# Optimization experiments

Hardware: AMD Instinct MI355X
Metric: run time of the kernel (lower is better)

Reference implementation:

```python
import jax, jax.numpy as jnp
import numpy as np
from jax import lax

C, CMID, RED, SCALE, KUP, KENC = 128, 64, 8, 2, 5, 3


def _conv(x, w, b=None, pad=0, groups=1):
    y = lax.conv_general_dilated(x, w, (1, 1), [(pad, pad), (pad, pad)],
                                 feature_group_count=groups,
                                 dimension_numbers=('NCHW', 'OIHW', 'NCHW'))
    if b is not None:
        y = y + b[None, :, None, None]
    return y


def setup_inputs() -> dict:
    key = jax.random.key(0)
    ks = jax.random.split(key, 8)
    s = 0.05
    return {
        'X': jax.random.normal(ks[0], (2, C, 64, 64), jnp.float32),
        'w3': jax.random.normal(ks[1], (CMID, C, 3, 3), jnp.float32) * s,
        'b3': jnp.zeros((CMID,), jnp.float32),
        'w5': jax.random.normal(ks[2], (CMID, C, 5, 5), jnp.float32) * s,
        'b5': jnp.zeros((CMID,), jnp.float32),
        'wa1': jax.random.normal(ks[3], (CMID // RED, CMID, 1, 1), jnp.float32) * s,
        'ba1': jnp.zeros((CMID // RED,), jnp.float32),
        'wa2': jax.random.normal(ks[4], (CMID, CMID // RED, 1, 1), jnp.float32) * s,
        'ba2': jnp.zeros((CMID,), jnp.float32),
        'wedge': jax.random.normal(ks[5], (CMID, 1, 3, 3), jnp.float32) * s,
        'wenc': jax.random.normal(ks[6], ((SCALE * KUP) ** 2, CMID, KENC, KENC), jnp.float32) * s,
    }


def reference(X, w3, b3, w5, b5, wa1, ba1, wa2, ba2, wedge, wenc):
    b, c, h, w = X.shape
    h_, w_ = h * SCALE, w * SCALE

    # kernel-prediction branch: 3x3 + 5x5 compression convs
    W = _conv(X, w3, b3, pad=1) + _conv(X, w5, b5, pad=2)

    # DetailEnhanceAttention: SE-style channel gate + depthwise edge conv
    avg = jnp.mean(W, axis=(2, 3), keepdims=True)            # (b, cmid, 1, 1)
    a = _conv(avg, wa1, ba1, pad=0)
    a = jax.nn.sigmoid(_conv(a, wa2, ba2, pad=0))
    edge = _conv(W, wedge, None, pad=1, groups=CMID)          # depthwise 3x3
    W = W * a + edge

    # encoder conv -> (b, (scale*k_up)^2, h, w)
    W = _conv(W, wenc, None, pad=KENC // 2)

    # PixelShuffle(scale): channels (k_up^2, r, r) -> (k_up^2, h*r, w*r)
    Wp = W.reshape(b, KUP * KUP, SCALE, SCALE, h, w)
    Wp = Wp.transpose(0, 1, 4, 2, 5, 3).reshape(b, KUP * KUP, h_, w_)
    Wp = jax.nn.softmax(Wp, axis=1)                           # softmax over k_up^2 taps

    # nearest upsample of X to (b, c, h_, w_)
    Xu = jnp.repeat(jnp.repeat(X, SCALE, axis=2), SCALE, axis=3)

    # unfold: kernel=k_up, dilation=scale, padding=k_up//2*scale
    p = (KUP // 2) * SCALE
    Xpad = jnp.pad(Xu, ((0, 0), (0, 0), (p, p), (p, p)))
    # (b, c, k_up^2, h_, w_), tap index = ki*k_up + kj (torch unfold order)
    patches = jnp.stack([
        Xpad[:, :, i * SCALE:i * SCALE + h_, j * SCALE:j * SCALE + w_]
        for i in range(KUP) for j in range(KUP)
    ], axis=2)

    out = jnp.einsum('bkhw,bckhw->bchw', Wp, patches)
    return out
```

## Files before the change

### kernel.cpp

```cpp
#include <hip/hip_runtime.h>
#include <math.h>

typedef __attribute__((ext_vector_type(2))) _Float16 f16x2;
typedef __attribute__((ext_vector_type(4))) _Float16 f16x4;
typedef __attribute__((ext_vector_type(8))) _Float16 f16x8;
typedef __attribute__((ext_vector_type(4))) float f32x4;

#if __has_builtin(__builtin_amdgcn_fdot2)
#define FDOT2(a, b, c) __builtin_amdgcn_fdot2((a), (b), (c), false)
#else
static __device__ __forceinline__ float FDOT2(f16x2 a, f16x2 b, float c) {
  return c + (float)a[0] * (float)b[0] + (float)a[1] * (float)b[1];
}
#endif

#define XPAD8_B  0
#define WFC_B    2506752
#define WFE_B    2916352
#define WFEATP_B 3045376
#define WEDGET_B 4194304
#define BCOMB_B  4195456
#define AVG_B    4195712

__global__ __launch_bounds__(256) void prep_kernel(
    const float* __restrict__ X,
    const float* __restrict__ w3, const float* __restrict__ b3,
    const float* __restrict__ w5, const float* __restrict__ b5,
    const float* __restrict__ wedge, const float* __restrict__ wenc,
    char* __restrict__ wsb) {
  int idx = blockIdx.x * 256 + threadIdx.x;
  if (idx < 156672) {
    int x = idx % 72;
    int t = idx / 72;
    int y = t % 68;
    int t2 = t / 68;
    int gg = t2 & 15, b = t2 >> 4;
    int yy = y - 2, xx = x - 2;
    bool ok = (yy >= 0 && yy < 64 && xx >= 0 && xx < 64);
    f16x8 h;
#pragma unroll
    for (int j = 0; j < 8; ++j) {
      float v = ok ? X[((b * 128 + gg * 8 + j) << 12) + yy * 64 + xx] : 0.f;
      h[j] = (_Float16)v;
    }
    ((f16x8*)(wsb + XPAD8_B))[idx] = h;
  }
  if (idx < 25600) {
    int l = idx & 63;
    int q = idx >> 6;
    int ntg = q & 3;
    int q2 = q >> 2;
    int cc = q2 & 3;
    int t = q2 >> 2;
    int ky = t / 5, kx = t % 5;
    int oc = ntg * 16 + (l & 15);
    int ci0 = cc * 32 + (l >> 4) * 8;
    f16x8 h;
#pragma unroll
    for (int i = 0; i < 8; ++i) {
      int ci = ci0 + i;
      float v = w5[(oc * 128 + ci) * 25 + t];
      if (ky >= 1 && ky <= 3 && kx >= 1 && kx <= 3)
        v += w3[(oc * 128 + ci) * 9 + (ky - 1) * 3 + (kx - 1)];
      h[i] = (_Float16)v;
    }
    ((f16x8*)(wsb + WFC_B))[idx] = h;
  }
  if (idx < 8064) {
    int l = idx & 63;
    int q = idx >> 6;
    int nt = q % 7;
    int q2 = q / 7;
    int cc = q2 & 1;
    int t = q2 >> 1;
    int oc = nt * 16 + (l & 15);
    int ci0 = cc * 32 + (l >> 4) * 8;
    f16x8 h;
#pragma unroll
    for (int i = 0; i < 8; ++i) {
      float v = (oc < 100) ? wenc[(oc * 64 + ci0 + i) * 9 + t] : 0.f;
      h[i] = (_Float16)v;
    }
    ((f16x8*)(wsb + WFE_B))[idx] = h;
  }
  if (idx < 6272) {
    int plane = idx / 392, p = idx % 392;
    int r, c;
    if (p < 136) {
      r = (p >= 68) ? 65 : 0;
      c = p % 68;
    } else {
      int q = p - 136;
      r = 1 + (q >> 2);
      int cm = q & 3;
      c = (cm == 0) ? 0 : (64 + cm);
    }
    f16x8 z = {(_Float16)0.f, (_Float16)0.f, (_Float16)0.f, (_Float16)0.f,
               (_Float16)0.f, (_Float16)0.f, (_Float16)0.f, (_Float16)0.f};
    *(f16x8*)((_Float16*)(wsb + WFEATP_B) + ((size_t)(plane * 66 + r) * 68 + c) * 8) = z;
  }
  if (idx < 72) {
    int k = idx >> 3, gg = idx & 7;
    f16x8 h;
#pragma unroll
    for (int j = 0; j < 8; ++j) h[j] = (_Float16)wedge[(gg * 8 + j) * 9 + k];
    ((f16x8*)(wsb + WEDGET_B))[idx] = h;
  }
  if (idx < 64) ((float*)(wsb + BCOMB_B))[idx] = b3[idx] + b5[idx];
  if (idx < 128) ((float*)(wsb + AVG_B))[idx] = b3[idx & 63] + b5[idx & 63];
}

__global__ __launch_bounds__(256) void convw_kernel(
    const _Float16* __restrict__ xpad8, const f16x8* __restrict__ wfc,
    const float* __restrict__ bcomb, _Float16* __restrict__ wfeatp,
    float* __restrict__ avg) {
  __shared__ __attribute__((aligned(16))) _Float16 xs[18560];
  __shared__ float red[64];
  const int tid = threadIdx.x;
  const int z = blockIdx.z;
  const int b = z >> 2, ntg = z & 3;
  const int tx0 = blockIdx.x * 8, ty0 = blockIdx.y * 8;

  for (int u = tid; u < 2304; u += 256) {
    int gg = u / 144;
    int rem = u - gg * 144;
    int r = rem / 12, c = rem - r * 12;
    f16x8 v = *(const f16x8*)&xpad8[((size_t)((b * 16 + gg) * 68 + ty0 + r) * 72 + tx0 + c) * 8];
    *(f16x8*)&xs[gg * 1160 + r * 96 + c * 8] = v;
  }
  __syncthreads();

  const int w = __builtin_amdgcn_readfirstlane(tid >> 6);
  const int l = tid & 63;
  const int lm = l & 15, lg = l >> 4;
  const int p = w * 16 + lm;
  const int abase = (p >> 3) * 96 + (p & 7) * 8;

  f32x4 accA = {0.f, 0.f, 0.f, 0.f}, accB = {0.f, 0.f, 0.f, 0.f};
  for (int dy = 0; dy < 5; ++dy) {
    for (int dx = 0; dx < 5; ++dx) {
      const int t = dy * 5 + dx;
      const int toff = abase + dy * 96 + dx * 8;
      const f16x8* wt = wfc + (t * 16 + ntg) * 64 + l;
#pragma unroll
      for (int cc = 0; cc < 4; ++cc) {
        f16x8 a = *(const f16x8*)&xs[(cc * 4 + lg) * 1160 + toff];
        f16x8 bb = wt[cc * 256];
        if (cc & 1)
          accB = __builtin_amdgcn_mfma_f32_16x16x32_f16(a, bb, accB, 0, 0, 0);
        else
          accA = __builtin_amdgcn_mfma_f32_16x16x32_f16(a, bb, accA, 0, 0, 0);
      }
    }
  }
  f32x4 acc = accA + accB;

  float s = acc[0] + acc[1] + acc[2] + acc[3];
  s += __shfl_xor(s, 16);
  s += __shfl_xor(s, 32);
  const float bias = bcomb[ntg * 16 + lm];
  __syncthreads();
#pragma unroll
  for (int r = 0; r < 4; ++r) {
    int pd = w * 16 + lg * 4 + r;
    xs[pd * 24 + lm] = (_Float16)(acc[r] + bias);
  }
  if (l < 16) red[w * 16 + lm] = s;
  __syncthreads();
  if (tid < 128) {
    int g2 = tid >> 6, pd = tid & 63;
    f16x8 v = *(const f16x8*)&xs[pd * 24 + g2 * 8];
    int gy = ty0 + (pd >> 3), gx = tx0 + (pd & 7);
    *(f16x8*)&wfeatp[((size_t)((b * 8 + ntg * 2 + g2) * 66 + 1 + gy) * 68 + 1 + gx) * 8] = v;
  }
  if (tid < 16) {
    float tot = red[tid] + red[16 + tid] + red[32 + tid] + red[48 + tid];
    atomicAdd(&avg[b * 64 + ntg * 16 + tid], tot * (1.f / 4096.f));
  }
}

#define SM_XT  0
#define SM_XSV 26880
#define SM_TS  34688
#define SM_SML 34688
#define SM_SMW 49536
#define SM_TOT 57216

__global__ __launch_bounds__(512) void enccarafe_kernel(
    const _Float16* __restrict__ wfeatp, const f16x8* __restrict__ wfe,
    const _Float16* __restrict__ xpad8, const f16x8* __restrict__ wedgeT,
    const float* __restrict__ wa1, const float* __restrict__ ba1,
    const float* __restrict__ wa2, const float* __restrict__ ba2,
    const float* __restrict__ avg, float* __restrict__ out) {
  __shared__ __attribute__((aligned(16))) char smem[SM_TOT];
  __shared__ f16x8 wedt[72];
  __shared__ float tlat[8];
  __shared__ float gsh[64];
  _Float16* xt = (_Float16*)(smem + SM_XT);
  _Float16* xsv = (_Float16*)(smem + SM_XSV);
  _Float16* ts = (_Float16*)(smem + SM_TS);
  float* sml = (float*)(smem + SM_SML);
  f16x2* smw2 = (f16x2*)(smem + SM_SMW);

  const int tid = threadIdx.x;
  const int b = blockIdx.z;
  const int tx0 = blockIdx.x * 8, ty0 = blockIdx.y * 4;

  for (int u = tid; u < 1664; u += 512) {
    int gg = u / 104;
    int rem = u - gg * 104;
    int r = rem / 13, c = rem - r * 13;
    f16x8 v = *(const f16x8*)&xpad8[((size_t)((b * 16 + gg) * 68 + ty0 + r) * 72 + tx0 + c) * 8];
    *(f16x8*)&xt[gg * 840 + r * 104 + c * 8] = v;
  }
  for (int u = tid; u < 768; u += 512) {
    int gg = u / 96;
    int rem = u - gg * 96;
    int r = rem / 12, c = rem - r * 12;
    int pr = ty0 - 1 + r, pc = tx0 - 1 + c;
    f16x8 v = {(_Float16)0.f, (_Float16)0.f, (_Float16)0.f, (_Float16)0.f,
               (_Float16)0.f, (_Float16)0.f, (_Float16)0.f, (_Float16)0.f};
    if (pr >= 0 && pr < 66 && pc >= 0 && pc < 68)
      v = *(const f16x8*)&wfeatp[((size_t)((b * 8 + gg) * 66 + pr) * 68 + pc) * 8];
    *(f16x8*)&ts[gg * 776 + r * 96 + c * 8] = v;
  }
  if (tid < 72) wedt[tid] = wedgeT[tid];
  if (tid < 8) {
    float s = ba1[tid];
    for (int i = 0; i < 64; ++i) s += wa1[tid * 64 + i] * avg[b * 64 + i];
    tlat[tid] = s;
  }
  __syncthreads();
  if (tid < 64) {
    float s = ba2[tid];
#pragma unroll
    for (int j = 0; j < 8; ++j) s += wa2[tid * 8 + j] * tlat[j];
    gsh[tid] = 1.f / (1.f + expf(-s));
  }
  __syncthreads();

  for (int u = tid; u < 480; u += 512) {
    int gg = u / 60;
    int rem = u - gg * 60;
    int r6 = rem / 10, c10 = rem - r6 * 10;
    int vy = ty0 - 1 + r6, vx = tx0 - 1 + c10;
    f16x8 res = {(_Float16)0.f, (_Float16)0.f, (_Float16)0.f, (_Float16)0.f,
                 (_Float16)0.f, (_Float16)0.f, (_Float16)0.f, (_Float16)0.f};
    if (vy >= 0 && vy < 64 && vx >= 0 && vx < 64) {
      float vout[8];
      f16x8 ctr = *(const f16x8*)&ts[gg * 776 + (r6 + 1) * 96 + (c10 + 1) * 8];
#pragma unroll
      for (int j = 0; j < 8; ++j) vout[j] = (float)ctr[j] * gsh[gg * 8 + j];
#pragma unroll
      for (int ky = 0; ky < 3; ++ky) {
#pragma unroll
        for (int kx = 0; kx < 3; ++kx) {
          int k = ky * 3 + kx;
          f16x8 tv = *(const f16x8*)&ts[gg * 776 + (r6 + ky) * 96 + (c10 + kx) * 8];
          f16x8 wv = wedt[k * 8 + gg];
#pragma unroll
          for (int j = 0; j < 8; ++j) vout[j] = fmaf((float)wv[j], (float)tv[j], vout[j]);
        }
      }
#pragma unroll
      for (int j = 0; j < 8; ++j) res[j] = (_Float16)vout[j];
    }
    *(f16x8*)&xsv[gg * 488 + r6 * 80 + c10 * 8] = res;
  }
  __syncthreads();

  {
    const int w = __builtin_amdgcn_readfirstlane(tid >> 6);
    const int l = tid & 63;
    const int pg = w & 1, hs = w >> 1;
    const int lm = l & 15, lg = l >> 4;
    const int p = pg * 16 + lm;
    const int abase = (p >> 3) * 80 + (p & 7) * 8;
    const int nt0 = hs * 2;
    const int ncnt = (hs == 3) ? 1 : 2;

    f32x4 a0 = {0.f, 0.f, 0.f, 0.f}, a1 = {0.f, 0.f, 0.f, 0.f};
    for (int dy = 0; dy < 3; ++dy) {
      for (int dx = 0; dx < 3; ++dx) {
        const int t = dy * 3 + dx;
        const int toff = abase + dy * 80 + dx * 8;
#pragma unroll
        for (int cc = 0; cc < 2; ++cc) {
          f16x8 a = *(const f16x8*)&xsv[(cc * 4 + lg) * 488 + toff];
          f16x8 b0 = wfe[((t * 2 + cc) * 7 + nt0) * 64 + l];
          a0 = __builtin_amdgcn_mfma_f32_16x16x32_f16(a, b0, a0, 0, 0, 0);
          if (ncnt == 2) {
            f16x8 b1 = wfe[((t * 2 + cc) * 7 + nt0 + 1) * 64 + l];
            a1 = __builtin_amdgcn_mfma_f32_16x16x32_f16(a, b1, a1, 0, 0, 0);
          }
        }
      }
    }
#pragma unroll
    for (int r = 0; r < 4; ++r) {
      int pd = pg * 16 + 4 * lg + r;
      sml[pd * 116 + nt0 * 16 + lm] = a0[r];
      if (ncnt == 2) sml[pd * 116 + (nt0 + 1) * 16 + lm] = a1[r];
    }
  }
  __syncthreads();

  if (tid < 128) {
    int pix = tid >> 2, sub = tid & 3;
    float lv[25];
    float m = -1e30f;
#pragma unroll
    for (int k = 0; k < 25; ++k) {
      lv[k] = sml[pix * 116 + k * 4 + sub];
      m = fmaxf(m, lv[k]);
    }
    float s = 0.f;
#pragma unroll
    for (int k = 0; k < 25; ++k) {
      lv[k] = __expf(lv[k] - m);
      s += lv[k];
    }
    float inv = 1.f / s;
#pragma unroll
    for (int ki = 0; ki < 5; ++ki) {
#pragma unroll
      for (int pr = 0; pr < 3; ++pr) {
        float wlo = lv[ki * 5 + 2 * pr] * inv;
        float whi = (2 * pr + 1 < 5) ? lv[ki * 5 + 2 * pr + 1] * inv : 0.f;
        f16x2 pk = {(_Float16)wlo, (_Float16)whi};
        smw2[((ki * 3 + pr) * 32 + pix) * 4 + sub] = pk;
      }
    }
  }
  __syncthreads();

  {
    const int slot = tid >> 5, pix = tid & 31;
    const int py = pix >> 3, px = pix & 7;
    const _Float16* xb = xt + slot * 840;

    float acc[4][8];
#pragma unroll
    for (int s = 0; s < 4; ++s)
#pragma unroll
      for (int j = 0; j < 8; ++j) acc[s][j] = 0.f;

    union U8 { f16x8 v; unsigned int u[4]; };
#pragma unroll
    for (int ki = 0; ki < 5; ++ki) {
      const _Float16* row = xb + (py + ki) * 104 + px * 8;
      U8 C[6];
#pragma unroll
      for (int c = 0; c < 6; ++c) C[c].v = *(const f16x8*)(row + c * 8);
#pragma unroll
      for (int pr = 0; pr < 3; ++pr) {
        const f16x2* wp = &smw2[((ki * 3 + pr) * 32 + pix) * 4];
        f16x2 w0 = wp[0], w1 = wp[1], w2 = wp[2], w3 = wp[3];
        const U8& A = C[2 * pr];
        const U8& B = C[2 * pr + 1];
#pragma unroll
        for (int k = 0; k < 4; ++k) {
          unsigned int lo = __builtin_amdgcn_perm(B.u[k], A.u[k], 0x05040100u);
          unsigned int hi = __builtin_amdgcn_perm(B.u[k], A.u[k], 0x07060302u);
          f16x2 xlo = __builtin_bit_cast(f16x2, lo);
          f16x2 xhi = __builtin_bit_cast(f16x2, hi);
          acc[0][2 * k] = FDOT2(w0, xlo, acc[0][2 * k]);
          acc[1][2 * k] = FDOT2(w1, xlo, acc[1][2 * k]);
          acc[2][2 * k] = FDOT2(w2, xlo, acc[2][2 * k]);
          acc[3][2 * k] = FDOT2(w3, xlo, acc[3][2 * k]);
          acc[0][2 * k + 1] = FDOT2(w0, xhi, acc[0][2 * k + 1]);
          acc[1][2 * k + 1] = FDOT2(w1, xhi, acc[1][2 * k + 1]);
          acc[2][2 * k + 1] = FDOT2(w2, xhi, acc[2][2 * k + 1]);
          acc[3][2 * k + 1] = FDOT2(w3, xhi, acc[3][2 * k + 1]);
        }
      }
    }
    int y0o = 2 * (ty0 + py), x0o = 2 * (tx0 + px);
#pragma unroll
    for (int j = 0; j < 8; ++j) {
      int c = slot * 8 + j;
      float* op = out + ((size_t)(b * 128 + c) * 128 + y0o) * 128 + x0o;
      float2 v0 = {acc[0][j], acc[1][j]};
      float2 v1 = {acc[2][j], acc[3][j]};
      *(float2*)op = v0;
      *(float2*)(op + 128) = v1;
    }
  }
}

extern "C" void kernel_launch(void* const* d_in, const int* in_sizes, int n_in,
                              void* d_out, int out_size, void* d_ws, size_t ws_size,
                              hipStream_t stream) {
  const float* X     = (const float*)d_in[0];
  const float* w3    = (const float*)d_in[1];
  const float* b3    = (const float*)d_in[2];
  const float* w5    = (const float*)d_in[3];
  const float* b5    = (const float*)d_in[4];
  const float* wa1   = (const float*)d_in[5];
  const float* ba1   = (const float*)d_in[6];
  const float* wa2   = (const float*)d_in[7];
  const float* ba2   = (const float*)d_in[8];
  const float* wedge = (const float*)d_in[9];
  const float* wenc  = (const float*)d_in[10];
  char* wsb = (char*)d_ws;
  float* out = (float*)d_out;

  _Float16* xpad8  = (_Float16*)(wsb + XPAD8_B);
  f16x8*    wfc    = (f16x8*)(wsb + WFC_B);
  f16x8*    wfe    = (f16x8*)(wsb + WFE_B);
  _Float16* wfeatp = (_Float16*)(wsb + WFEATP_B);
  f16x8*    wedgeT = (f16x8*)(wsb + WEDGET_B);
  float*    bcomb  = (float*)(wsb + BCOMB_B);
  float*    avg    = (float*)(wsb + AVG_B);

  prep_kernel<<<612, 256, 0, stream>>>(X, w3, b3, w5, b5, wedge, wenc, wsb);
  convw_kernel<<<dim3(8, 8, 8), 256, 0, stream>>>(xpad8, wfc, bcomb, wfeatp, avg);
  enccarafe_kernel<<<dim3(8, 16, 2), 512, 0, stream>>>(
      wfeatp, wfe, xpad8, wedgeT, wa1, ba1, wa2, ba2, avg, out);
}
```

Baseline: 47.65 us.

## Restructure convw: all output channels per block with split-K across waves

After: 48.84 us. 1.02x slower.

```diff
diff --git a/kernel.cpp b/kernel.cpp
--- a/kernel.cpp
+++ b/kernel.cpp
@@ -110,72 +110,97 @@
   if (idx < 128) ((float*)(wsb + AVG_B))[idx] = b3[idx & 63] + b5[idx & 63];
 }
 
-__global__ __launch_bounds__(256) void convw_kernel(
+__global__ __launch_bounds__(512) void convw_kernel(
     const _Float16* __restrict__ xpad8, const f16x8* __restrict__ wfc,
     const float* __restrict__ bcomb, _Float16* __restrict__ wfeatp,
     float* __restrict__ avg) {
-  __shared__ __attribute__((aligned(16))) _Float16 xs[18560];
-  __shared__ float red[64];
+  __shared__ __attribute__((aligned(16))) _Float16 xs[16 * 776];
+  __shared__ float red[4][64][8];
+  __shared__ float redm[2][2][2][16];
   const int tid = threadIdx.x;
-  const int z = blockIdx.z;
-  const int b = z >> 2, ntg = z & 3;
-  const int tx0 = blockIdx.x * 8, ty0 = blockIdx.y * 8;
-
-  for (int u = tid; u < 2304; u += 256) {
-    int gg = u / 144;
-    int rem = u - gg * 144;
+  const int b = blockIdx.z;
+  const int tx0 = blockIdx.x * 8, ty0 = blockIdx.y * 4;
+
+  for (int u = tid; u < 1536; u += 512) {
+    int gg = u / 96;
+    int rem = u - gg * 96;
     int r = rem / 12, c = rem - r * 12;
     f16x8 v = *(const f16x8*)&xpad8[((size_t)((b * 16 + gg) * 68 + ty0 + r) * 72 + tx0 + c) * 8];
-    *(f16x8*)&xs[gg * 1160 + r * 96 + c * 8] = v;
+    *(f16x8*)&xs[gg * 776 + r * 96 + c * 8] = v;
   }
   __syncthreads();
 
   const int w = __builtin_amdgcn_readfirstlane(tid >> 6);
   const int l = tid & 63;
+  const int pg = w & 1, ocp = (w >> 1) & 1, kh = w >> 2;
   const int lm = l & 15, lg = l >> 4;
-  const int p = w * 16 + lm;
+  const int p = pg * 16 + lm;
   const int abase = (p >> 3) * 96 + (p & 7) * 8;
 
-  f32x4 accA = {0.f, 0.f, 0.f, 0.f}, accB = {0.f, 0.f, 0.f, 0.f};
+  f32x4 acc0 = {0.f, 0.f, 0.f, 0.f}, acc1 = {0.f, 0.f, 0.f, 0.f};
   for (int dy = 0; dy < 5; ++dy) {
     for (int dx = 0; dx < 5; ++dx) {
       const int t = dy * 5 + dx;
       const int toff = abase + dy * 96 + dx * 8;
-      const f16x8* wt = wfc + (t * 16 + ntg) * 64 + l;
-#pragma unroll
-      for (int cc = 0; cc < 4; ++cc) {
-        f16x8 a = *(const f16x8*)&xs[(cc * 4 + lg) * 1160 + toff];
-        f16x8 bb = wt[cc * 256];
-        if (cc & 1)
-          accB = __builtin_amdgcn_mfma_f32_16x16x32_f16(a, bb, accB, 0, 0, 0);
-        else
-          accA = __builtin_amdgcn_mfma_f32_16x16x32_f16(a, bb, accA, 0, 0, 0);
+#pragma unroll
+      for (int cc2 = 0; cc2 < 2; ++cc2) {
+        const int cc = kh * 2 + cc2;
+        f16x8 a = *(const f16x8*)&xs[(cc * 4 + lg) * 776 + toff];
+        const f16x8* wt = wfc + ((t * 4 + cc) * 4 + ocp * 2) * 64 + l;
+        f16x8 b0 = wt[0];
+        f16x8 b1 = wt[64];
+        acc0 = __builtin_amdgcn_mfma_f32_16x16x32_f16(a, b0, acc0, 0, 0, 0);
+        acc1 = __builtin_amdgcn_mfma_f32_16x16x32_f16(a, b1, acc1, 0, 0, 0);
       }
     }
   }
-  f32x4 acc = accA + accB;
-
-  float s = acc[0] + acc[1] + acc[2] + acc[3];
-  s += __shfl_xor(s, 16);
-  s += __shfl_xor(s, 32);
-  const float bias = bcomb[ntg * 16 + lm];
-  __syncthreads();
-#pragma unroll
-  for (int r = 0; r < 4; ++r) {
-    int pd = w * 16 + lg * 4 + r;
-    xs[pd * 24 + lm] = (_Float16)(acc[r] + bias);
-  }
-  if (l < 16) red[w * 16 + lm] = s;
-  __syncthreads();
-  if (tid < 128) {
-    int g2 = tid >> 6, pd = tid & 63;
-    f16x8 v = *(const f16x8*)&xs[pd * 24 + g2 * 8];
+
+  if (kh == 1) {
+#pragma unroll
+    for (int r = 0; r < 4; ++r) {
+      red[pg * 2 + ocp][l][r] = acc0[r];
+      red[pg * 2 + ocp][l][4 + r] = acc1[r];
+    }
+  }
+  __syncthreads();
+  if (kh == 0) {
+#pragma unroll
+    for (int r = 0; r < 4; ++r) {
+      acc0[r] += red[pg * 2 + ocp][l][r];
+      acc1[r] += red[pg * 2 + ocp][l][4 + r];
+    }
+    float s0 = acc0[0] + acc0[1] + acc0[2] + acc0[3];
+    float s1 = acc1[0] + acc1[1] + acc1[2] + acc1[3];
+    s0 += __shfl_xor(s0, 16);
+    s0 += __shfl_xor(s0, 32);
+    s1 += __shfl_xor(s1, 16);
+    s1 += __shfl_xor(s1, 32);
+    if (lg == 0) {
+      redm[pg][ocp][0][lm] = s0;
+      redm[pg][ocp][1][lm] = s1;
+    }
+    const int oc0 = ocp * 32 + lm;
+    const float bias0 = bcomb[oc0];
+    const float bias1 = bcomb[oc0 + 16];
+    _Float16* xs2 = xs;
+#pragma unroll
+    for (int r = 0; r < 4; ++r) {
+      int pd = pg * 16 + lg * 4 + r;
+      xs2[pd * 80 + oc0] = (_Float16)(acc0[r] + bias0);
+      xs2[pd * 80 + oc0 + 16] = (_Float16)(acc1[r] + bias1);
+    }
+  }
+  __syncthreads();
+  if (tid < 256) {
+    int g2 = tid >> 5, pd = tid & 31;
+    f16x8 v = *(const f16x8*)&xs[pd * 80 + g2 * 8];
     int gy = ty0 + (pd >> 3), gx = tx0 + (pd & 7);
-    *(f16x8*)&wfeatp[((size_t)((b * 8 + ntg * 2 + g2) * 66 + 1 + gy) * 68 + 1 + gx) * 8] = v;
-  }
-  if (tid < 16) {
-    float tot = red[tid] + red[16 + tid] + red[32 + tid] + red[48 + tid];
-    atomicAdd(&avg[b * 64 + ntg * 16 + tid], tot * (1.f / 4096.f));
+    *(f16x8*)&wfeatp[((size_t)((b * 8 + g2) * 66 + 1 + gy) * 68 + 1 + gx) * 8] = v;
+  }
+  if (tid < 64) {
+    int ocpq = tid >> 5, ntl = (tid >> 4) & 1, lmq = tid & 15;
+    float tot = redm[0][ocpq][ntl][lmq] + redm[1][ocpq][ntl][lmq];
+    atomicAdd(&avg[b * 64 + tid], tot * (1.f / 4096.f));
   }
 }
 
@@ -414,7 +439,7 @@
   float*    avg    = (float*)(wsb + AVG_B);
 
   prep_kernel<<<612, 256, 0, stream>>>(X, w3, b3, w5, b5, wedge, wenc, wsb);
-  convw_kernel<<<dim3(8, 8, 8), 256, 0, stream>>>(xpad8, wfc, bcomb, wfeatp, avg);
+  convw_kernel<<<dim3(8, 16, 2), 512, 0, stream>>>(xpad8, wfc, bcomb, wfeatp, avg);
   enccarafe_kernel<<<dim3(8, 16, 2), 512, 0, stream>>>(
       wfeatp, wfe, xpad8, wedgeT, wa1, ba1, wa2, ba2, avg, out);
 }
```

## Fuse three kernels into one persistent kernel with software grid barriers

Applied to the files above, without the earlier changes.

Result: slower. 107.1 us (+124.8%).

```diff
diff --git a/kernel.cpp b/kernel.cpp
--- a/kernel.cpp
+++ b/kernel.cpp
@@ -21,162 +21,26 @@
 #define WEDGET_B 4194304
 #define BCOMB_B  4195456
 #define AVG_B    4195712
-
-__global__ __launch_bounds__(256) void prep_kernel(
-    const float* __restrict__ X,
-    const float* __restrict__ w3, const float* __restrict__ b3,
-    const float* __restrict__ w5, const float* __restrict__ b5,
-    const float* __restrict__ wedge, const float* __restrict__ wenc,
-    char* __restrict__ wsb) {
-  int idx = blockIdx.x * 256 + threadIdx.x;
-  if (idx < 156672) {
-    int x = idx % 72;
-    int t = idx / 72;
-    int y = t % 68;
-    int t2 = t / 68;
-    int gg = t2 & 15, b = t2 >> 4;
-    int yy = y - 2, xx = x - 2;
-    bool ok = (yy >= 0 && yy < 64 && xx >= 0 && xx < 64);
-    f16x8 h;
-#pragma unroll
-    for (int j = 0; j < 8; ++j) {
-      float v = ok ? X[((b * 128 + gg * 8 + j) << 12) + yy * 64 + xx] : 0.f;
-      h[j] = (_Float16)v;
-    }
-    ((f16x8*)(wsb + XPAD8_B))[idx] = h;
-  }
-  if (idx < 25600) {
-    int l = idx & 63;
-    int q = idx >> 6;
-    int ntg = q & 3;
-    int q2 = q >> 2;
-    int cc = q2 & 3;
-    int t = q2 >> 2;
-    int ky = t / 5, kx = t % 5;
-    int oc = ntg * 16 + (l & 15);
-    int ci0 = cc * 32 + (l >> 4) * 8;
-    f16x8 h;
-#pragma unroll
-    for (int i = 0; i < 8; ++i) {
-      int ci = ci0 + i;
-      float v = w5[(oc * 128 + ci) * 25 + t];
-      if (ky >= 1 && ky <= 3 && kx >= 1 && kx <= 3)
-        v += w3[(oc * 128 + ci) * 9 + (ky - 1) * 3 + (kx - 1)];
-      h[i] = (_Float16)v;
-    }
-    ((f16x8*)(wsb + WFC_B))[idx] = h;
-  }
-  if (idx < 8064) {
-    int l = idx & 63;
-    int q = idx >> 6;
-    int nt = q % 7;
-    int q2 = q / 7;
-    int cc = q2 & 1;
-    int t = q2 >> 1;
-    int oc = nt * 16 + (l & 15);
-    int ci0 = cc * 32 + (l >> 4) * 8;
-    f16x8 h;
-#pragma unroll
-    for (int i = 0; i < 8; ++i) {
-      float v = (oc < 100) ? wenc[(oc * 64 + ci0 + i) * 9 + t] : 0.f;
-      h[i] = (_Float16)v;
-    }
-    ((f16x8*)(wsb + WFE_B))[idx] = h;
-  }
-  if (idx < 6272) {
-    int plane = idx / 392, p = idx % 392;
-    int r, c;
-    if (p < 136) {
-      r = (p >= 68) ? 65 : 0;
-      c = p % 68;
+#define BAR_B    4196224
+
+static __device__ __forceinline__ void grid_barrier(unsigned int* bar, unsigned int nb) {
+  __syncthreads();
+  if (threadIdx.x == 0) {
+    __threadfence();
+    unsigned int* cnt = bar;
+    unsigned int* gen = bar + 1;
+    unsigned int g = atomicAdd(gen, 0u);
+    unsigned int a = atomicAdd(cnt, 1u);
+    if (a == nb - 1) {
+      atomicExch(cnt, 0u);
+      __threadfence();
+      atomicAdd(gen, 1u);
     } else {
-      int q = p - 136;
-      r = 1 + (q >> 2);
-      int cm = q & 3;
-      c = (cm == 0) ? 0 : (64 + cm);
-    }
-    f16x8 z = {(_Float16)0.f, (_Float16)0.f, (_Float16)0.f, (_Float16)0.f,
-               (_Float16)0.f, (_Float16)0.f, (_Float16)0.f, (_Float16)0.f};
-    *(f16x8*)((_Float16*)(wsb + WFEATP_B) + ((size_t)(plane * 66 + r) * 68 + c) * 8) = z;
-  }
-  if (idx < 72) {
-    int k = idx >> 3, gg = idx & 7;
-    f16x8 h;
-#pragma unroll
-    for (int j = 0; j < 8; ++j) h[j] = (_Float16)wedge[(gg * 8 + j) * 9 + k];
-    ((f16x8*)(wsb + WEDGET_B))[idx] = h;
-  }
-  if (idx < 64) ((float*)(wsb + BCOMB_B))[idx] = b3[idx] + b5[idx];
-  if (idx < 128) ((float*)(wsb + AVG_B))[idx] = b3[idx & 63] + b5[idx & 63];
-}
-
-__global__ __launch_bounds__(256) void convw_kernel(
-    const _Float16* __restrict__ xpad8, const f16x8* __restrict__ wfc,
-    const float* __restrict__ bcomb, _Float16* __restrict__ wfeatp,
-    float* __restrict__ avg) {
-  __shared__ __attribute__((aligned(16))) _Float16 xs[18560];
-  __shared__ float red[64];
-  const int tid = threadIdx.x;
-  const int z = blockIdx.z;
-  const int b = z >> 2, ntg = z & 3;
-  const int tx0 = blockIdx.x * 8, ty0 = blockIdx.y * 8;
-
-  for (int u = tid; u < 2304; u += 256) {
-    int gg = u / 144;
-    int rem = u - gg * 144;
-    int r = rem / 12, c = rem - r * 12;
-    f16x8 v = *(const f16x8*)&xpad8[((size_t)((b * 16 + gg) * 68 + ty0 + r) * 72 + tx0 + c) * 8];
-    *(f16x8*)&xs[gg * 1160 + r * 96 + c * 8] = v;
+      while (atomicAdd(gen, 0u) == g) __builtin_amdgcn_s_sleep(8);
+      __threadfence();
+    }
   }
   __syncthreads();
-
-  const int w = __builtin_amdgcn_readfirstlane(tid >> 6);
-  const int l = tid & 63;
-  const int lm = l & 15, lg = l >> 4;
-  const int p = w * 16 + lm;
-  const int abase = (p >> 3) * 96 + (p & 7) * 8;
-
-  f32x4 accA = {0.f, 0.f, 0.f, 0.f}, accB = {0.f, 0.f, 0.f, 0.f};
-  for (int dy = 0; dy < 5; ++dy) {
-    for (int dx = 0; dx < 5; ++dx) {
-      const int t = dy * 5 + dx;
-      const int toff = abase + dy * 96 + dx * 8;
-      const f16x8* wt = wfc + (t * 16 + ntg) * 64 + l;
-#pragma unroll
-      for (int cc = 0; cc < 4; ++cc) {
-        f16x8 a = *(const f16x8*)&xs[(cc * 4 + lg) * 1160 + toff];
-        f16x8 bb = wt[cc * 256];
-        if (cc & 1)
-          accB = __builtin_amdgcn_mfma_f32_16x16x32_f16(a, bb, accB, 0, 0, 0);
-        else
-          accA = __builtin_amdgcn_mfma_f32_16x16x32_f16(a, bb, accA, 0, 0, 0);
-      }
-    }
-  }
-  f32x4 acc = accA + accB;
-
-  float s = acc[0] + acc[1] + acc[2] + acc[3];
-  s += __shfl_xor(s, 16);
-  s += __shfl_xor(s, 32);
-  const float bias = bcomb[ntg * 16 + lm];
-  __syncthreads();
-#pragma unroll
-  for (int r = 0; r < 4; ++r) {
-    int pd = w * 16 + lg * 4 + r;
-    xs[pd * 24 + lm] = (_Float16)(acc[r] + bias);
-  }
-  if (l < 16) red[w * 16 + lm] = s;
-  __syncthreads();
-  if (tid < 128) {
-    int g2 = tid >> 6, pd = tid & 63;
-    f16x8 v = *(const f16x8*)&xs[pd * 24 + g2 * 8];
-    int gy = ty0 + (pd >> 3), gx = tx0 + (pd & 7);
-    *(f16x8*)&wfeatp[((size_t)((b * 8 + ntg * 2 + g2) * 66 + 1 + gy) * 68 + 1 + gx) * 8] = v;
-  }
-  if (tid < 16) {
-    float tot = red[tid] + red[16 + tid] + red[32 + tid] + red[48 + tid];
-    atomicAdd(&avg[b * 64 + ntg * 16 + tid], tot * (1.f / 4096.f));
-  }
 }
 
 #define SM_XT  0
@@ -184,206 +48,381 @@
 #define SM_TS  34688
 #define SM_SML 34688
 #define SM_SMW 49536
-#define SM_TOT 57216
-
-__global__ __launch_bounds__(512) void enccarafe_kernel(
-    const _Float16* __restrict__ wfeatp, const f16x8* __restrict__ wfe,
-    const _Float16* __restrict__ xpad8, const f16x8* __restrict__ wedgeT,
-    const float* __restrict__ wa1, const float* __restrict__ ba1,
-    const float* __restrict__ wa2, const float* __restrict__ ba2,
-    const float* __restrict__ avg, float* __restrict__ out) {
-  __shared__ __attribute__((aligned(16))) char smem[SM_TOT];
-  __shared__ f16x8 wedt[72];
-  __shared__ float tlat[8];
-  __shared__ float gsh[64];
-  _Float16* xt = (_Float16*)(smem + SM_XT);
-  _Float16* xsv = (_Float16*)(smem + SM_XSV);
-  _Float16* ts = (_Float16*)(smem + SM_TS);
-  float* sml = (float*)(smem + SM_SML);
-  f16x2* smw2 = (f16x2*)(smem + SM_SMW);
-
+#define SM_WED 57216
+#define SM_TLA 58368
+#define SM_GSH 58400
+
+__global__ __launch_bounds__(512) void fused_kernel(
+    const float* __restrict__ X, const float* __restrict__ w3,
+    const float* __restrict__ b3, const float* __restrict__ w5,
+    const float* __restrict__ b5, const float* __restrict__ wa1,
+    const float* __restrict__ ba1, const float* __restrict__ wa2,
+    const float* __restrict__ ba2, const float* __restrict__ wedge,
+    const float* __restrict__ wenc, char* __restrict__ wsb,
+    float* __restrict__ out) {
+  __shared__ __attribute__((aligned(16))) char SMEM[83968];
   const int tid = threadIdx.x;
-  const int b = blockIdx.z;
-  const int tx0 = blockIdx.x * 8, ty0 = blockIdx.y * 4;
-
-  for (int u = tid; u < 1664; u += 512) {
-    int gg = u / 104;
-    int rem = u - gg * 104;
-    int r = rem / 13, c = rem - r * 13;
-    f16x8 v = *(const f16x8*)&xpad8[((size_t)((b * 16 + gg) * 68 + ty0 + r) * 72 + tx0 + c) * 8];
-    *(f16x8*)&xt[gg * 840 + r * 104 + c * 8] = v;
+  const int bid = blockIdx.x;
+  unsigned int* bar = (unsigned int*)(wsb + BAR_B);
+
+  {
+    for (int idx = bid * 512 + tid; idx < 156672; idx += 131072) {
+      int x = idx % 72;
+      int t = idx / 72;
+      int y = t % 68;
+      int t2 = t / 68;
+      int gg = t2 & 15, b = t2 >> 4;
+      int yy = y - 2, xx = x - 2;
+      bool ok = (yy >= 0 && yy < 64 && xx >= 0 && xx < 64);
+      f16x8 h;
+#pragma unroll
+      for (int j = 0; j < 8; ++j) {
+        float v = ok ? X[((b * 128 + gg * 8 + j) << 12) + yy * 64 + xx] : 0.f;
+        h[j] = (_Float16)v;
+      }
+      ((f16x8*)(wsb + XPAD8_B))[idx] = h;
+    }
+    int idx = bid * 512 + tid;
+    if (idx < 25600) {
+      int l = idx & 63;
+      int q = idx >> 6;
+      int ntg = q & 3;
+      int q2 = q >> 2;
+      int cc = q2 & 3;
+      int t = q2 >> 2;
+      int ky = t / 5, kx = t % 5;
+      int oc = ntg * 16 + (l & 15);
+      int ci0 = cc * 32 + (l >> 4) * 8;
+      f16x8 h;
+#pragma unroll
+      for (int i = 0; i < 8; ++i) {
+        int ci = ci0 + i;
+        float v = w5[(oc * 128 + ci) * 25 + t];
+        if (ky >= 1 && ky <= 3 && kx >= 1 && kx <= 3)
+          v += w3[(oc * 128 + ci) * 9 + (ky - 1) * 3 + (kx - 1)];
+        h[i] = (_Float16)v;
+      }
+      ((f16x8*)(wsb + WFC_B))[idx] = h;
+    }
+    if (idx < 8064) {
+      int l = idx & 63;
+      int q = idx >> 6;
+      int nt = q % 7;
+      int q2 = q / 7;
+      int cc = q2 & 1;
+      int t = q2 >> 1;
+      int oc = nt * 16 + (l & 15);
+      int ci0 = cc * 32 + (l >> 4) * 8;
+      f16x8 h;
+#pragma unroll
+      for (int i = 0; i < 8; ++i) {
+        float v = (oc < 100) ? wenc[(oc * 64 + ci0 + i) * 9 + t] : 0.f;
+        h[i] = (_Float16)v;
+      }
+      ((f16x8*)(wsb + WFE_B))[idx] = h;
+    }
+    if (idx < 6272) {
+      int plane = idx / 392, p = idx % 392;
+      int r, c;
+      if (p < 136) {
+        r = (p >= 68) ? 65 : 0;
+        c = p % 68;
+      } else {
+        int q = p - 136;
+        r = 1 + (q >> 2);
+        int cm = q & 3;
+        c = (cm == 0) ? 0 : (64 + cm);
+      }
+      f16x8 z = {(_Float16)0.f, (_Float16)0.f, (_Float16)0.f, (_Float16)0.f,
+                 (_Float16)0.f, (_Float16)0.f, (_Float16)0.f, (_Float16)0.f};
+      *(f16x8*)((_Float16*)(wsb + WFEATP_B) + ((size_t)(plane * 66 + r) * 68 + c) * 8) = z;
+    }
+    if (idx < 72) {
+      int k = idx >> 3, gg = idx & 7;
+      f16x8 h;
+#pragma unroll
+      for (int j = 0; j < 8; ++j) h[j] = (_Float16)wedge[(gg * 8 + j) * 9 + k];
+      ((f16x8*)(wsb + WEDGET_B))[idx] = h;
+    }
+    if (idx < 64) ((float*)(wsb + BCOMB_B))[idx] = b3[idx] + b5[idx];
+    if (idx < 128) ((float*)(wsb + AVG_B))[idx] = b3[idx & 63] + b5[idx & 63];
   }
-  for (int u = tid; u < 768; u += 512) {
-    int gg = u / 96;
-    int rem = u - gg * 96;
-    int r = rem / 12, c = rem - r * 12;
-    int pr = ty0 - 1 + r, pc = tx0 - 1 + c;
-    f16x8 v = {(_Float16)0.f, (_Float16)0.f, (_Float16)0.f, (_Float16)0.f,
-               (_Float16)0.f, (_Float16)0.f, (_Float16)0.f, (_Float16)0.f};
-    if (pr >= 0 && pr < 66 && pc >= 0 && pc < 68)
-      v = *(const f16x8*)&wfeatp[((size_t)((b * 8 + gg) * 66 + pr) * 68 + pc) * 8];
-    *(f16x8*)&ts[gg * 776 + r * 96 + c * 8] = v;
+  grid_barrier(bar, 256);
+
+  {
+    const _Float16* xpad8 = (const _Float16*)(wsb + XPAD8_B);
+    const f16x8* wfc = (const f16x8*)(wsb + WFC_B);
+    const float* bcomb = (const float*)(wsb + BCOMB_B);
+    _Float16* wfeatp = (_Float16*)(wsb + WFEATP_B);
+    float* avg = (float*)(wsb + AVG_B);
+
+    const int half = tid >> 8;
+    const int t2 = tid & 255;
+    const int u = bid * 2 + half;
+    const int bx = u & 7, byy = (u >> 3) & 7, zz = u >> 6;
+    const int b = zz >> 2, ntg = zz & 3;
+    const int tx0 = bx * 8, ty0 = byy * 8;
+    _Float16* xs = (_Float16*)(SMEM + half * 37120);
+    float* red = (float*)(SMEM + 74240 + half * 256);
+
+    for (int uu = t2; uu < 2304; uu += 256) {
+      int gg = uu / 144;
+      int rem = uu - gg * 144;
+      int r = rem / 12, c = rem - r * 12;
+      f16x8 v = *(const f16x8*)&xpad8[((size_t)((b * 16 + gg) * 68 + ty0 + r) * 72 + tx0 + c) * 8];
+      *(f16x8*)&xs[gg * 1160 + r * 96 + c * 8] = v;
+    }
+    __syncthreads();
+
+    const int w = __builtin_amdgcn_readfirstlane(t2 >> 6);
+    const int l = t2 & 63;
+    const int lm = l & 15, lg = l >> 4;
+    const int p = w * 16 + lm;
+    const int abase = (p >> 3) * 96 + (p & 7) * 8;
+
+    f32x4 accA = {0.f, 0.f, 0.f, 0.f}, accB = {0.f, 0.f, 0.f, 0.f};
+    for (int dy = 0; dy < 5; ++dy) {
+      for (int dx = 0; dx < 5; ++dx) {
+        const int t = dy * 5 + dx;
+        const int toff = abase + dy * 96 + dx * 8;
+        const f16x8* wt = wfc + (t * 16 + ntg) * 64 + l;
+#pragma unroll
+        for (int cc = 0; cc < 4; ++cc) {
+          f16x8 a = *(const f16x8*)&xs[(cc * 4 + lg) * 1160 + toff];
+          f16x8 bb = wt[cc * 256];
+          if (cc & 1)
+            accB = __builtin_amdgcn_mfma_f32_16x16x32_f16(a, bb, accB, 0, 0, 0);
+          else
+            accA = __builtin_amdgcn_mfma_f32_16x16x32_f16(a, bb, accA, 0, 0, 0);
+        }
+      }
+    }
+    f32x4 acc = accA + accB;
+
+    float s = acc[0] + acc[1] + acc[2] + acc[3];
+    s += __shfl_xor(s, 16);
+    s += __shfl_xor(s, 32);
+    const float bias = bcomb[ntg * 16 + lm];
+    __syncthreads();
+#pragma unroll
+    for (int r = 0; r < 4; ++r) {
+      int pd = w * 16 + lg * 4 + r;
+      xs[pd * 24 + lm] = (_Float16)(acc[r] + bias);
+    }
+    if (l < 16) red[w * 16 + lm] = s;
+    __syncthreads();
+    if (t2 < 128) {
+      int g2 = t2 >> 6, pd = t2 & 63;
+      f16x8 v = *(const f16x8*)&xs[pd * 24 + g2 * 8];
+      int gy = ty0 + (pd >> 3), gx = tx0 + (pd & 7);
+      *(f16x8*)&wfeatp[((size_t)((b * 8 + ntg * 2 + g2) * 66 + 1 + gy) * 68 + 1 + gx) * 8] = v;
+    }
+    if (t2 < 16) {
+      float tot = red[t2] + red[16 + t2] + red[32 + t2] + red[48 + t2];
+      atomicAdd(&avg[b * 64 + ntg * 16 + t2], tot * (1.f / 4096.f));
+    }
   }
-  if (tid < 72) wedt[tid] = wedgeT[tid];
-  if (tid < 8) {
-    float s = ba1[tid];
-    for (int i = 0; i < 64; ++i) s += wa1[tid * 64 + i] * avg[b * 64 + i];
-    tlat[tid] = s;
-  }
-  __syncthreads();
-  if (tid < 64) {
-    float s = ba2[tid];
-#pragma unroll
-    for (int j = 0; j < 8; ++j) s += wa2[tid * 8 + j] * tlat[j];
-    gsh[tid] = 1.f / (1.f + expf(-s));
-  }
-  __syncthreads();
-
-  for (int u = tid; u < 480; u += 512) {
-    int gg = u / 60;
-    int rem = u - gg * 60;
-    int r6 = rem / 10, c10 = rem - r6 * 10;
-    int vy = ty0 - 1 + r6, vx = tx0 - 1 + c10;
-    f16x8 res = {(_Float16)0.f, (_Float16)0.f, (_Float16)0.f, (_Float16)0.f,
+  grid_barrier(bar, 256);
+
+  {
+    const _Float16* wfeatp = (const _Float16*)(wsb + WFEATP_B);
+    const f16x8* wfe = (const f16x8*)(wsb + WFE_B);
+    const _Float16* xpad8 = (const _Float16*)(wsb + XPAD8_B);
+    const f16x8* wedgeT = (const f16x8*)(wsb + WEDGET_B);
+    const float* avg = (const float*)(wsb + AVG_B);
+
+    _Float16* xt = (_Float16*)(SMEM + SM_XT);
+    _Float16* xsv = (_Float16*)(SMEM + SM_XSV);
+    _Float16* ts = (_Float16*)(SMEM + SM_TS);
+    float* sml = (float*)(SMEM + SM_SML);
+    f16x2* smw2 = (f16x2*)(SMEM + SM_SMW);
+    f16x8* wedt = (f16x8*)(SMEM + SM_WED);
+    float* tlat = (float*)(SMEM + SM_TLA);
+    float* gsh = (float*)(SMEM + SM_GSH);
+
+    const int b = bid >> 7;
+    const int byy = (bid >> 3) & 15, bx = bid & 7;
+    const int tx0 = bx * 8, ty0 = byy * 4;
+
+    for (int u = tid; u < 1664; u += 512) {
+      int gg = u / 104;
+      int rem = u - gg * 104;
+      int r = rem / 13, c = rem - r * 13;
+      f16x8 v = *(const f16x8*)&xpad8[((size_t)((b * 16 + gg) * 68 + ty0 + r) * 72 + tx0 + c) * 8];
+      *(f16x8*)&xt[gg * 840 + r * 104 + c * 8] = v;
+    }
+    for (int u = tid; u < 768; u += 512) {
+      int gg = u / 96;
+      int rem = u - gg * 96;
+      int r = rem / 12, c = rem - r * 12;
+      int pr = ty0 - 1 + r, pc = tx0 - 1 + c;
+      f16x8 v = {(_Float16)0.f, (_Float16)0.f, (_Float16)0.f, (_Float16)0.f,
                  (_Float16)0.f, (_Float16)0.f, (_Float16)0.f, (_Float16)0.f};
-    if (vy >= 0 && vy < 64 && vx >= 0 && vx < 64) {
-      float vout[8];
-      f16x8 ctr = *(const f16x8*)&ts[gg * 776 + (r6 + 1) * 96 + (c10 + 1) * 8];
-#pragma unroll
-      for (int j = 0; j < 8; ++j) vout[j] = (float)ctr[j] * gsh[gg * 8 + j];
-#pragma unroll
-      for (int ky = 0; ky < 3; ++ky) {
-#pragma unroll
-        for (int kx = 0; kx < 3; ++kx) {
-          int k = ky * 3 + kx;
-          f16x8 tv = *(const f16x8*)&ts[gg * 776 + (r6 + ky) * 96 + (c10 + kx) * 8];
-          f16x8 wv = wedt[k * 8 + gg];
-#pragma unroll
-          for (int j = 0; j < 8; ++j) vout[j] = fmaf((float)wv[j], (float)tv[j], vout[j]);
-        }
-      }
-#pragma unroll
-      for (int j = 0; j < 8; ++j) res[j] = (_Float16)vout[j];
-    }
-    *(f16x8*)&xsv[gg * 488 + r6 * 80 + c10 * 8] = res;
-  }
-  __syncthreads();
-
-  {
-    const int w = __builtin_amdgcn_readfirstlane(tid >> 6);
-    const int l = tid & 63;
-    const int pg = w & 1, hs = w >> 1;
-    const int lm = l & 15, lg = l >> 4;
-    const int p = pg * 16 + lm;
-    const int abase = (p >> 3) * 80 + (p & 7) * 8;
-    const int nt0 = hs * 2;
-    const int ncnt = (hs == 3) ? 1 : 2;
-
-    f32x4 a0 = {0.f, 0.f, 0.f, 0.f}, a1 = {0.f, 0.f, 0.f, 0.f};
-    for (int dy = 0; dy < 3; ++dy) {
-      for (int dx = 0; dx < 3; ++dx) {
-        const int t = dy * 3 + dx;
-        const int toff = abase + dy * 80 + dx * 8;
-#pragma unroll
-        for (int cc = 0; cc < 2; ++cc) {
-          f16x8 a = *(const f16x8*)&xsv[(cc * 4 + lg) * 488 + toff];
-          f16x8 b0 = wfe[((t * 2 + cc) * 7 + nt0) * 64 + l];
-          a0 = __builtin_amdgcn_mfma_f32_16x16x32_f16(a, b0, a0, 0, 0, 0);
-          if (ncnt == 2) {
-            f16x8 b1 = wfe[((t * 2 + cc) * 7 + nt0 + 1) * 64 + l];
-            a1 = __builtin_amdgcn_mfma_f32_16x16x32_f16(a, b1, a1, 0, 0, 0);
+      if (pr >= 0 && pr < 66 && pc >= 0 && pc < 68)
+        v = *(const f16x8*)&wfeatp[((size_t)((b * 8 + gg) * 66 + pr) * 68 + pc) * 8];
+      *(f16x8*)&ts[gg * 776 + r * 96 + c * 8] = v;
+    }
+    if (tid < 72) wedt[tid] = wedgeT[tid];
+    if (tid < 8) {
+      float s = ba1[tid];
+      for (int i = 0; i < 64; ++i) s += wa1[tid * 64 + i] * avg[b * 64 + i];
+      tlat[tid] = s;
+    }
+    __syncthreads();
+    if (tid < 64) {
+      float s = ba2[tid];
+#pragma unroll
+      for (int j = 0; j < 8; ++j) s += wa2[tid * 8 + j] * tlat[j];
+      gsh[tid] = 1.f / (1.f + expf(-s));
+    }
+    __syncthreads();
+
+    for (int u = tid; u < 480; u += 512) {
+      int gg = u / 60;
+      int rem = u - gg * 60;
+      int r6 = rem / 10, c10 = rem - r6 * 10;
+      int vy = ty0 - 1 + r6, vx = tx0 - 1 + c10;
+      f16x8 res = {(_Float16)0.f, (_Float16)0.f, (_Float16)0.f, (_Float16)0.f,
+                   (_Float16)0.f, (_Float16)0.f, (_Float16)0.f, (_Float16)0.f};
+      if (vy >= 0 && vy < 64 && vx >= 0 && vx < 64) {
+        float vout[8];
+        f16x8 ctr = *(const f16x8*)&ts[gg * 776 + (r6 + 1) * 96 + (c10 + 1) * 8];
+#pragma unroll
+        for (int j = 0; j < 8; ++j) vout[j] = (float)ctr[j] * gsh[gg * 8 + j];
+#pragma unroll
+        for (int ky = 0; ky < 3; ++ky) {
+#pragma unroll
+          for (int kx = 0; kx < 3; ++kx) {
+            int k = ky * 3 + kx;
+            f16x8 tv = *(const f16x8*)&ts[gg * 776 + (r6 + ky) * 96 + (c10 + kx) * 8];
+            f16x8 wv = wedt[k * 8 + gg];
+#pragma unroll
+            for (int j = 0; j < 8; ++j) vout[j] = fmaf((float)wv[j], (float)tv[j], vout[j]);
           }
         }
-      }
-    }
-#pragma unroll
-    for (int r = 0; r < 4; ++r) {
-      int pd = pg * 16 + 4 * lg + r;
-      sml[pd * 116 + nt0 * 16 + lm] = a0[r];
-      if (ncnt == 2) sml[pd * 116 + (nt0 + 1) * 16 + lm] = a1[r];
-    }
-  }
-  __syncthreads();
-
-  if (tid < 128) {
-    int pix = tid >> 2, sub = tid & 3;
-    float lv[25];
-    float m = -1e30f;
-#pragma unroll
-    for (int k = 0; k < 25; ++k) {
-      lv[k] = sml[pix * 116 + k * 4 + sub];
-      m = fmaxf(m, lv[k]);
-    }
-    float s = 0.f;
-#pragma unroll
-    for (int k = 0; k < 25; ++k) {
-      lv[k] = __expf(lv[k] - m);
-      s += lv[k];
-    }
-    float inv = 1.f / s;
-#pragma unroll
-    for (int ki = 0; ki < 5; ++ki) {
-#pragma unroll
-      for (int pr = 0; pr < 3; ++pr) {
-        float wlo = lv[ki * 5 + 2 * pr] * inv;
-        float whi = (2 * pr + 1 < 5) ? lv[ki * 5 + 2 * pr + 1] * inv : 0.f;
-        f16x2 pk = {(_Float16)wlo, (_Float16)whi};
-        smw2[((ki * 3 + pr) * 32 + pix) * 4 + sub] = pk;
-      }
-    }
-  }
-  __syncthreads();
-
-  {
-    const int slot = tid >> 5, pix = tid & 31;
-    const int py = pix >> 3, px = pix & 7;
-    const _Float16* xb = xt + slot * 840;
-
-    float acc[4][8];
-#pragma unroll
-    for (int s = 0; s < 4; ++s)
-#pragma unroll
-      for (int j = 0; j < 8; ++j) acc[s][j] = 0.f;
-
-    union U8 { f16x8 v; unsigned int u[4]; };
-#pragma unroll
-    for (int ki = 0; ki < 5; ++ki) {
-      const _Float16* row = xb + (py + ki) * 104 + px * 8;
-      U8 C[6];
-#pragma unroll
-      for (int c = 0; c < 6; ++c) C[c].v = *(const f16x8*)(row + c * 8);
-#pragma unroll
-      for (int pr = 0; pr < 3; ++pr) {
-        const f16x2* wp = &smw2[((ki * 3 + pr) * 32 + pix) * 4];
-        f16x2 w0 = wp[0], w1 = wp[1], w2 = wp[2], w3 = wp[3];
-        const U8& A = C[2 * pr];
-        const U8& B = C[2 * pr + 1];
-#pragma unroll
-        for (int k = 0; k < 4; ++k) {
-          unsigned int lo = __builtin_amdgcn_perm(B.u[k], A.u[k], 0x05040100u);
-          unsigned int hi = __builtin_amdgcn_perm(B.u[k], A.u[k], 0x07060302u);
-          f16x2 xlo = __builtin_bit_cast(f16x2, lo);
-          f16x2 xhi = __builtin_bit_cast(f16x2, hi);
-          acc[0][2 * k] = FDOT2(w0, xlo, acc[0][2 * k]);
-          acc[1][2 * k] = FDOT2(w1, xlo, acc[1][2 * k]);
-          acc[2][2 * k] = FDOT2(w2, xlo, acc[2][2 * k]);
-          acc[3][2 * k] = FDOT2(w3, xlo, acc[3][2 * k]);
-          acc[0][2 * k + 1] = FDOT2(w0, xhi, acc[0][2 * k + 1]);
-          acc[1][2 * k + 1] = FDOT2(w1, xhi, acc[1][2 * k + 1]);
-          acc[2][2 * k + 1] = FDOT2(w2, xhi, acc[2][2 * k + 1]);
-          acc[3][2 * k + 1] = FDOT2(w3, xhi, acc[3][2 * k + 1]);
+#pragma unroll
+        for (int j = 0; j < 8; ++j) res[j] = (_Float16)vout[j];
+      }
+      *(f16x8*)&xsv[gg * 488 + r6 * 80 + c10 * 8] = res;
+    }
+    __syncthreads();
+
+    {
+      const int w = __builtin_amdgcn_readfirstlane(tid >> 6);
+      const int l = tid & 63;
+      const int pg = w & 1, hs = w >> 1;
+      const int lm = l & 15, lg = l >> 4;
+      const int p = pg * 16 + lm;
+      const int abase = (p >> 3) * 80 + (p & 7) * 8;
+      const int nt0 = hs * 2;
+      const int ncnt = (hs == 3) ? 1 : 2;
+
+      f32x4 a0 = {0.f, 0.f, 0.f, 0.f}, a1 = {0.f, 0.f, 0.f, 0.f};
+      for (int dy = 0; dy < 3; ++dy) {
+        for (int dx = 0; dx < 3; ++dx) {
+          const int t = dy * 3 + dx;
+          const int toff = abase + dy * 80 + dx * 8;
+#pragma unroll
+          for (int cc = 0; cc < 2; ++cc) {
+            f16x8 a = *(const f16x8*)&xsv[(cc * 4 + lg) * 488 + toff];
+            f16x8 b0 = wfe[((t * 2 + cc) * 7 + nt0) * 64 + l];
+            a0 = __builtin_amdgcn_mfma_f32_16x16x32_f16(a, b0, a0, 0, 0, 0);
+            if (ncnt == 2) {
+              f16x8 b1 = wfe[((t * 2 + cc) * 7 + nt0 + 1) * 64 + l];
+              a1 = __builtin_amdgcn_mfma_f32_16x16x32_f16(a, b1, a1, 0, 0, 0);
+            }
+          }
         }
       }
-    }
-    int y0o = 2 * (ty0 + py), x0o = 2 * (tx0 + px);
-#pragma unroll
-    for (int j = 0; j < 8; ++j) {
-      int c = slot * 8 + j;
-      float* op = out + ((size_t)(b * 128 + c) * 128 + y0o) * 128 + x0o;
-      float2 v0 = {acc[0][j], acc[1][j]};
-      float2 v1 = {acc[2][j], acc[3][j]};
-      *(float2*)op = v0;
-      *(float2*)(op + 128) = v1;
+#pragma unroll
+      for (int r = 0; r < 4; ++r) {
+        int pd = pg * 16 + 4 * lg + r;
+        sml[pd * 116 + nt0 * 16 + lm] = a0[r];
+        if (ncnt == 2) sml[pd * 116 + (nt0 + 1) * 16 + lm] = a1[r];
+      }
+    }
+    __syncthreads();
+
+    if (tid < 128) {
+      int pix = tid >> 2, sub = tid & 3;
+      float lv[25];
+      float m = -1e30f;
+#pragma unroll
+      for (int k = 0; k < 25; ++k) {
+        lv[k] = sml[pix * 116 + k * 4 + sub];
+        m = fmaxf(m, lv[k]);
+      }
+      float s = 0.f;
+#pragma unroll
+      for (int k = 0; k < 25; ++k) {
+        lv[k] = __expf(lv[k] - m);
+        s += lv[k];
+      }
+      float inv = 1.f / s;
+#pragma unroll
+      for (int ki = 0; ki < 5; ++ki) {
+#pragma unroll
+        for (int pr = 0; pr < 3; ++pr) {
+          float wlo = lv[ki * 5 + 2 * pr] * inv;
+          float whi = (2 * pr + 1 < 5) ? lv[ki * 5 + 2 * pr + 1] * inv : 0.f;
+          f16x2 pk = {(_Float16)wlo, (_Float16)whi};
+          smw2[((ki * 3 + pr) * 32 + pix) * 4 + sub] = pk;
+        }
+      }
+    }
+    __syncthreads();
+
+    {
+      const int slot = tid >> 5, pix = tid & 31;
+      const int py = pix >> 3, px = pix & 7;
+      const _Float16* xb = xt + slot * 840;
+
+      float acc[4][8];
+#pragma unroll
+      for (int s = 0; s < 4; ++s)
+#pragma unroll
+        for (int j = 0; j < 8; ++j) acc[s][j] = 0.f;
+
+      union U8 { f16x8 v; unsigned int u[4]; };
+#pragma unroll
+      for (int ki = 0; ki < 5; ++ki) {
+        const _Float16* row = xb + (py + ki) * 104 + px * 8;
+        U8 C[6];
+#pragma unroll
+        for (int c = 0; c < 6; ++c) C[c].v = *(const f16x8*)(row + c * 8);
+#pragma unroll
+        for (int pr = 0; pr < 3; ++pr) {
+          const f16x2* wp = &smw2[((ki * 3 + pr) * 32 + pix) * 4];
+          f16x2 w0 = wp[0], w1 = wp[1], w2 = wp[2], w3 = wp[3];
+          const U8& A = C[2 * pr];
+          const U8& B = C[2 * pr + 1];
+#pragma unroll
+          for (int k = 0; k < 4; ++k) {
+            unsigned int lo = __builtin_amdgcn_perm(B.u[k], A.u[k], 0x05040100u);
+            unsigned int hi = __builtin_amdgcn_perm(B.u[k], A.u[k], 0x07060302u);
+            f16x2 xlo = __builtin_bit_cast(f16x2, lo);
+            f16x2 xhi = __builtin_bit_cast(f16x2, hi);
+            acc[0][2 * k] = FDOT2(w0, xlo, acc[0][2 * k]);
+            acc[1][2 * k] = FDOT2(w1, xlo, acc[1][2 * k]);
+            acc[2][2 * k] = FDOT2(w2, xlo, acc[2][2 * k]);
+            acc[3][2 * k] = FDOT2(w3, xlo, acc[3][2 * k]);
+            acc[0][2 * k + 1] = FDOT2(w0, xhi, acc[0][2 * k + 1]);
+            acc[1][2 * k + 1] = FDOT2(w1, xhi, acc[1][2 * k + 1]);
+            acc[2][2 * k + 1] = FDOT2(w2, xhi, acc[2][2 * k + 1]);
+            acc[3][2 * k + 1] = FDOT2(w3, xhi, acc[3][2 * k + 1]);
+          }
+        }
+      }
+      int y0o = 2 * (ty0 + py), x0o = 2 * (tx0 + px);
+#pragma unroll
+      for (int j = 0; j < 8; ++j) {
+        int c = slot * 8 + j;
+        float* op = out + ((size_t)(b * 128 + c) * 128 + y0o) * 128 + x0o;
+        float2 v0 = {acc[0][j], acc[1][j]};
+        float2 v1 = {acc[2][j], acc[3][j]};
+        *(float2*)op = v0;
+        *(float2*)(op + 128) = v1;
+      }
     }
   }
 }
@@ -405,16 +444,7 @@
   char* wsb = (char*)d_ws;
   float* out = (float*)d_out;
 
-  _Float16* xpad8  = (_Float16*)(wsb + XPAD8_B);
-  f16x8*    wfc    = (f16x8*)(wsb + WFC_B);
-  f16x8*    wfe    = (f16x8*)(wsb + WFE_B);
-  _Float16* wfeatp = (_Float16*)(wsb + WFEATP_B);
-  f16x8*    wedgeT = (f16x8*)(wsb + WEDGET_B);
-  float*    bcomb  = (float*)(wsb + BCOMB_B);
-  float*    avg    = (float*)(wsb + AVG_B);
-
-  prep_kernel<<<612, 256, 0, stream>>>(X, w3, b3, w5, b5, wedge, wenc, wsb);
-  convw_kernel<<<dim3(8, 8, 8), 256, 0, stream>>>(xpad8, wfc, bcomb, wfeatp, avg);
-  enccarafe_kernel<<<dim3(8, 16, 2), 512, 0, stream>>>(
-      wfeatp, wfe, xpad8, wedgeT, wa1, ba1, wa2, ba2, avg, out);
+  hipMemsetAsync(wsb + BAR_B, 0, 8, stream);
+  fused_kernel<<<256, 512, 0, stream>>>(X, w3, b3, w5, b5, wa1, ba1, wa2, ba2,
+                                        wedge, wenc, wsb, out);
 }
```
